# Kernel tuning notes

Hardware: AMD Instinct MI355X
Metric: run time of the kernel (lower is better)

Reference implementation:

```python
import jax, jax.numpy as jnp
import numpy as np

D = 512      # dim_model
F = 2048     # dim_feedforward
E = 8        # num_experts
K = 2        # num_experts_per_token
B, S = 2, 4096


def setup_inputs() -> dict:
    key = jax.random.key(0)
    ks = jax.random.split(key, 8)
    sd = 1.0 / np.sqrt(D)
    sf = 1.0 / np.sqrt(F)
    return {
        "x": jax.random.normal(ks[0], (B, S, D), dtype=jnp.float32),
        "router_w": jax.random.uniform(ks[1], (D, E), jnp.float32, -sd, sd),
        "router_b": jax.random.uniform(ks[2], (E,), jnp.float32, -sd, sd),
        "w1": jax.random.uniform(ks[3], (E, D, F), jnp.float32, -sd, sd),
        "b1": jax.random.uniform(ks[4], (E, F), jnp.float32, -sd, sd),
        "w2": jax.random.uniform(ks[5], (E, F, D), jnp.float32, -sf, sf),
        "b2": jax.random.uniform(ks[6], (E, D), jnp.float32, -sf, sf),
    }


def reference(x, router_w, router_b, w1, b1, w2, b2):
    orig_shape = x.shape
    flat = x.reshape(-1, orig_shape[-1])                     # [T, D]
    logits = flat @ router_w + router_b                      # [T, E]
    gates = jax.nn.softmax(logits, axis=-1)                  # [T, E]
    top_vals, top_idx = jax.lax.top_k(gates, K)              # [T, K]
    top_vals = top_vals / jnp.sum(top_vals, axis=-1, keepdims=True)
    # combine weight per (token, expert): zero for unselected experts,
    # so dense per-expert evaluation yields identical math to masked dispatch.
    onehot = jax.nn.one_hot(top_idx, E, dtype=flat.dtype)    # [T, K, E]
    comb = jnp.einsum('tk,tke->te', top_vals, onehot)        # [T, E]
    # expert FFNs over all tokens (dropout is identity in eval)
    hidden = jax.nn.relu(jnp.einsum('td,edf->etf', flat, w1) + b1[:, None, :])  # [E, T, F]
    eout = jnp.einsum('etf,efd->etd', hidden, w2) + b2[:, None, :]              # [E, T, D]
    out = jnp.einsum('te,etd->td', comb, eout)               # [T, D]
    return out.reshape(orig_shape)
```

## Files before the change

### kernel.cpp

```cpp
#include <hip/hip_runtime.h>
#include <cstdint>
#include <cstddef>

#define TD 512
#define TF 2048
#define NE 8
#define NT 8192
#define CAP 17408

using u16 = unsigned short;
using u32 = unsigned int;

typedef __attribute__((ext_vector_type(8))) __bf16 bf16x8;
typedef __attribute__((ext_vector_type(4))) float f32x4;

__device__ __forceinline__ u16 f2bf(float f) {
  u32 u = __float_as_uint(f);
  u32 r = (u + 0x7fffu + ((u >> 16) & 1u)) >> 16;
  return (u16)r;
}

__device__ __forceinline__ float bf2f(u16 b) {
  return __uint_as_float((u32)b << 16);
}

__device__ __forceinline__ void load_lds16(const void* g, void* l) {
  __builtin_amdgcn_global_load_lds(
      (const __attribute__((address_space(1))) void*)g,
      (__attribute__((address_space(3))) void*)l, 16, 0, 0);
}

__global__ void transpose_cvt_kernel(const float* __restrict__ in, u16* __restrict__ out,
                                     int R, int C) {
  __shared__ u16 tile[32][33];
  int c0 = blockIdx.x * 32, r0 = blockIdx.y * 32;
  const float* ib = in + (size_t)blockIdx.z * R * C;
  u16* ob = out + (size_t)blockIdx.z * R * C;
  #pragma unroll
  for (int rr = 0; rr < 32; rr += 8) {
    int r = r0 + threadIdx.y + rr;
    int c = c0 + threadIdx.x;
    tile[threadIdx.y + rr][threadIdx.x] = f2bf(ib[(size_t)r * C + c]);
  }
  __syncthreads();
  #pragma unroll
  for (int rr = 0; rr < 32; rr += 8) {
    int oc = c0 + threadIdx.y + rr;
    int orr = r0 + threadIdx.x;
    ob[(size_t)oc * R + orr] = tile[threadIdx.x][threadIdx.y + rr];
  }
}

__global__ void router_kernel(const float* __restrict__ x, const float* __restrict__ rw,
                              const float* __restrict__ rb, int2* __restrict__ tokE,
                              float2* __restrict__ tokG, u16* __restrict__ xb) {
  int wv = threadIdx.x >> 6;
  int lane = threadIdx.x & 63;
  int t = blockIdx.x * 4 + wv;
  const float* xr = x + (size_t)t * TD;
  float4 a0 = *reinterpret_cast<const float4*>(xr + lane * 4);
  float4 a1 = *reinterpret_cast<const float4*>(xr + 256 + lane * 4);
  {
    u16 o[8];
    o[0] = f2bf(a0.x); o[1] = f2bf(a0.y); o[2] = f2bf(a0.z); o[3] = f2bf(a0.w);
    o[4] = f2bf(a1.x); o[5] = f2bf(a1.y); o[6] = f2bf(a1.z); o[7] = f2bf(a1.w);
    u16* xo = xb + (size_t)t * TD;
    *reinterpret_cast<uint2*>(xo + lane * 4) = *reinterpret_cast<uint2*>(o);
    *reinterpret_cast<uint2*>(xo + 256 + lane * 4) = *reinterpret_cast<uint2*>(o + 4);
  }
  float p[NE];
  #pragma unroll
  for (int e = 0; e < NE; e++) p[e] = 0.f;
  float av[8] = {a0.x, a0.y, a0.z, a0.w, a1.x, a1.y, a1.z, a1.w};
  #pragma unroll
  for (int j = 0; j < 8; j++) {
    int d = (j < 4) ? (lane * 4 + j) : (256 + lane * 4 + j - 4);
    const float* r = rw + (size_t)d * NE;
    #pragma unroll
    for (int e = 0; e < NE; e++) p[e] += av[j] * r[e];
  }
  #pragma unroll
  for (int off = 32; off >= 1; off >>= 1) {
    #pragma unroll
    for (int e = 0; e < NE; e++) p[e] += __shfl_xor(p[e], off);
  }
  if (lane == 0) {
    float l[NE];
    #pragma unroll
    for (int e = 0; e < NE; e++) l[e] = p[e] + rb[e];
    float m = l[0];
    #pragma unroll
    for (int e = 1; e < NE; e++) m = fmaxf(m, l[e]);
    float g[NE];
    #pragma unroll
    for (int e = 0; e < NE; e++) g[e] = __expf(l[e] - m);
    int i0 = 0;
    #pragma unroll
    for (int e = 1; e < NE; e++) if (g[e] > g[i0]) i0 = e;
    int i1 = -1;
    #pragma unroll
    for (int e = 0; e < NE; e++) {
      if (e == i0) continue;
      if (i1 < 0 || g[e] > g[i1]) i1 = e;
    }
    float inv = 1.f / (g[i0] + g[i1]);
    tokE[t] = make_int2(i0, i1);
    tokG[t] = make_float2(g[i0] * inv, g[i1] * inv);
  }
}

__global__ void count_offsets_kernel(const int2* __restrict__ tokE, int* __restrict__ offs,
                                     int* __restrict__ cursors) {
  __shared__ int hist[NE];
  if (threadIdx.x < NE) {
    hist[threadIdx.x] = 0;
    cursors[threadIdx.x * 16] = 0;
  }
  __syncthreads();
  for (int t = threadIdx.x; t < NT; t += 1024) {
    int2 e = tokE[t];
    atomicAdd(&hist[e.x], 1);
    atomicAdd(&hist[e.y], 1);
  }
  __syncthreads();
  if (threadIdx.x == 0) {
    int tot = 0;
    for (int e = 0; e < NE; e++) {
      offs[e] = tot;
      tot += (hist[e] + 127) & ~127;
    }
    offs[NE] = tot;
  }
}

__global__ void fill_kernel(const int* __restrict__ offs, int* __restrict__ tok,
                            int* __restrict__ sexp) {
  int s = blockIdx.x * 256 + threadIdx.x;
  int e = NE - 1;
  #pragma unroll
  for (int i = 0; i < NE; i++)
    if (s >= offs[i] && s < offs[i + 1]) e = i;
  sexp[s] = e;
  tok[s] = -1;
}

__global__ void scatter_kernel(const int2* __restrict__ tokE,
                               const int* __restrict__ offs, int* __restrict__ cursors,
                               int* __restrict__ tok, int* __restrict__ slotOf) {
  int t = blockIdx.x * 256 + threadIdx.x;
  int lane = threadIdx.x & 63;
  int2 e = tokE[t];
  #pragma unroll
  for (int k = 0; k < 2; k++) {
    int ek = k ? e.y : e.x;
    #pragma unroll
    for (int ex = 0; ex < NE; ex++) {
      unsigned long long mask = __ballot(ek == ex);
      if (ek == ex) {
        int leader = __ffsll(mask) - 1;
        int rank = __popcll(mask & ((1ull << lane) - 1ull));
        int base = 0;
        if (lane == leader) base = atomicAdd(&cursors[ex * 16], __popcll(mask));
        base = __shfl(base, leader);
        int s = offs[ex] + base + rank;
        tok[s] = t;
        slotOf[t * 2 + k] = s;
      }
    }
  }
}

__global__ __launch_bounds__(256, 3) void gemm1_kernel(
    const u16* __restrict__ xb, const u16* __restrict__ w1t,
    const float* __restrict__ b1, const int* __restrict__ tok,
    const int* __restrict__ sexp, u16* __restrict__ H) {
  __shared__ u16 As[128 * 64];
  __shared__ u16 Bs[128 * 64];
  __shared__ int tokS[128];
  const int tid = threadIdx.x;
  const int s0 = blockIdx.x * 128;
  const int f0 = blockIdx.y * 128;
  const int e = sexp[s0];
  if (tid < 128) {
    int t = tok[s0 + tid];
    tokS[tid] = t < 0 ? 0 : t;
  }
  __syncthreads();

  const int lane = tid & 63;
  const int wv = tid >> 6;
  const int srow = lane >> 3;
  const int scol = (((lane & 7) ^ srow) & 7) * 8;
  const int wm = (wv >> 1) * 64;
  const int wn = (wv & 1) * 64;
  const int mrow = lane & 15;
  const int quad = lane >> 4;
  const int rq = mrow & 7;

  f32x4 zero = {0.f, 0.f, 0.f, 0.f};
  f32x4 acc[4][4];
  #pragma unroll
  for (int i = 0; i < 4; i++)
    #pragma unroll
    for (int j = 0; j < 4; j++) acc[i][j] = zero;

  const u16* bbase = w1t + ((size_t)e * TF + f0) * TD;

  for (int k0 = 0; k0 < TD; k0 += 64) {
    if (k0) __syncthreads();
    #pragma unroll
    for (int p = 0; p < 4; p++) {
      int row = wv * 32 + p * 8 + srow;
      load_lds16(xb + (size_t)tokS[row] * TD + k0 + scol, &As[(wv * 32 + p * 8) * 64]);
      load_lds16(bbase + (size_t)row * TD + k0 + scol, &Bs[(wv * 32 + p * 8) * 64]);
    }
    __syncthreads();
    #pragma unroll
    for (int ks = 0; ks < 2; ks++) {
      bf16x8 a[4], b[4];
      #pragma unroll
      for (int i = 0; i < 4; i++)
        a[i] = *reinterpret_cast<const bf16x8*>(
            &As[(wm + i * 16 + mrow) * 64 + ((ks * 4 + quad) ^ rq) * 8]);
      #pragma unroll
      for (int j = 0; j < 4; j++)
        b[j] = *reinterpret_cast<const bf16x8*>(
            &Bs[(wn + j * 16 + mrow) * 64 + ((ks * 4 + quad) ^ rq) * 8]);
      #pragma unroll
      for (int i = 0; i < 4; i++)
        #pragma unroll
        for (int j = 0; j < 4; j++)
          acc[i][j] = __builtin_amdgcn_mfma_f32_16x16x32_bf16(a[i], b[j], acc[i][j], 0, 0, 0);
    }
  }

  float bv[4];
  #pragma unroll
  for (int j = 0; j < 4; j++) bv[j] = b1[e * TF + f0 + wn + j * 16 + mrow];
  #pragma unroll
  for (int i = 0; i < 4; i++) {
    #pragma unroll
    for (int r = 0; r < 4; r++) {
      int row = s0 + wm + i * 16 + quad * 4 + r;
      u16* hrow = H + (size_t)row * TF + f0;
      #pragma unroll
      for (int j = 0; j < 4; j++) {
        float v = acc[i][j][r] + bv[j];
        v = v > 0.f ? v : 0.f;
        hrow[wn + j * 16 + mrow] = f2bf(v);
      }
    }
  }
}

__global__ __launch_bounds__(256, 3) void gemm2_kernel(
    const u16* __restrict__ H, const u16* __restrict__ w2t,
    const float* __restrict__ b2, const int* __restrict__ sexp,
    u16* __restrict__ eout) {
  __shared__ u16 As[128 * 64];
  __shared__ u16 Bs[128 * 64];
  const int tid = threadIdx.x;
  const int s0 = blockIdx.x * 128;
  const int d0 = blockIdx.y * 128;
  const int e = sexp[s0];

  const int lane = tid & 63;
  const int wv = tid >> 6;
  const int srow = lane >> 3;
  const int scol = (((lane & 7) ^ srow) & 7) * 8;
  const int wm = (wv >> 1) * 64;
  const int wn = (wv & 1) * 64;
  const int mrow = lane & 15;
  const int quad = lane >> 4;
  const int rq = mrow & 7;

  f32x4 zero = {0.f, 0.f, 0.f, 0.f};
  f32x4 acc[4][4];
  #pragma unroll
  for (int i = 0; i < 4; i++)
    #pragma unroll
    for (int j = 0; j < 4; j++) acc[i][j] = zero;

  const u16* bbase = w2t + ((size_t)e * TD + d0) * TF;

  for (int k0 = 0; k0 < TF; k0 += 64) {
    if (k0) __syncthreads();
    #pragma unroll
    for (int p = 0; p < 4; p++) {
      int row = wv * 32 + p * 8 + srow;
      load_lds16(H + (size_t)(s0 + row) * TF + k0 + scol, &As[(wv * 32 + p * 8) * 64]);
      load_lds16(bbase + (size_t)row * TF + k0 + scol, &Bs[(wv * 32 + p * 8) * 64]);
    }
    __syncthreads();
    #pragma unroll
    for (int ks = 0; ks < 2; ks++) {
      bf16x8 a[4], b[4];
      #pragma unroll
      for (int i = 0; i < 4; i++)
        a[i] = *reinterpret_cast<const bf16x8*>(
            &As[(wm + i * 16 + mrow) * 64 + ((ks * 4 + quad) ^ rq) * 8]);
      #pragma unroll
      for (int j = 0; j < 4; j++)
        b[j] = *reinterpret_cast<const bf16x8*>(
            &Bs[(wn + j * 16 + mrow) * 64 + ((ks * 4 + quad) ^ rq) * 8]);
      #pragma unroll
      for (int i = 0; i < 4; i++)
        #pragma unroll
        for (int j = 0; j < 4; j++)
          acc[i][j] = __builtin_amdgcn_mfma_f32_16x16x32_bf16(a[i], b[j], acc[i][j], 0, 0, 0);
    }
  }

  float bv[4];
  #pragma unroll
  for (int j = 0; j < 4; j++) bv[j] = b2[e * TD + d0 + wn + j * 16 + mrow];
  #pragma unroll
  for (int i = 0; i < 4; i++) {
    #pragma unroll
    for (int r = 0; r < 4; r++) {
      int row = s0 + wm + i * 16 + quad * 4 + r;
      u16* orow = eout + (size_t)row * TD + d0;
      #pragma unroll
      for (int j = 0; j < 4; j++) {
        orow[wn + j * 16 + mrow] = f2bf(acc[i][j][r] + bv[j]);
      }
    }
  }
}

__global__ void combine_kernel(const u16* __restrict__ eout, const int* __restrict__ slotOf,
                               const float2* __restrict__ tokG, float* __restrict__ out) {
  int wv = threadIdx.x >> 6;
  int lane = threadIdx.x & 63;
  int t = blockIdx.x * 4 + wv;
  int sA = slotOf[t * 2];
  int sB = slotOf[t * 2 + 1];
  float2 g = tokG[t];
  uint4 ua = *reinterpret_cast<const uint4*>(eout + (size_t)sA * TD + lane * 8);
  uint4 ub = *reinterpret_cast<const uint4*>(eout + (size_t)sB * TD + lane * 8);
  const u16* pa = reinterpret_cast<const u16*>(&ua);
  const u16* pb = reinterpret_cast<const u16*>(&ub);
  float o[8];
  #pragma unroll
  for (int k = 0; k < 8; k++) o[k] = g.x * bf2f(pa[k]) + g.y * bf2f(pb[k]);
  float* od = out + (size_t)t * TD + lane * 8;
  *reinterpret_cast<float4*>(od) = make_float4(o[0], o[1], o[2], o[3]);
  *reinterpret_cast<float4*>(od + 4) = make_float4(o[4], o[5], o[6], o[7]);
}

extern "C" void kernel_launch(void* const* d_in, const int* in_sizes, int n_in,
                              void* d_out, int out_size, void* d_ws, size_t ws_size,
                              hipStream_t stream) {
  const float* x  = (const float*)d_in[0];
  const float* rw = (const float*)d_in[1];
  const float* rb = (const float*)d_in[2];
  const float* w1 = (const float*)d_in[3];
  const float* b1 = (const float*)d_in[4];
  const float* w2 = (const float*)d_in[5];
  const float* b2 = (const float*)d_in[6];
  float* out = (float*)d_out;

  char* w = (char*)d_ws;
  u16* xb   = (u16*)w;            w += (size_t)NT * TD * 2;
  u16* w1t  = (u16*)w;            w += (size_t)NE * TD * TF * 2;
  u16* w2t  = (u16*)w;            w += (size_t)NE * TF * TD * 2;
  u16* H    = (u16*)w;            w += (size_t)CAP * TF * 2;
  u16* eout = (u16*)w;            w += (size_t)CAP * TD * 2;
  int* tok  = (int*)w;            w += (size_t)CAP * 4;
  int* sexp = (int*)w;            w += (size_t)CAP * 4;
  int* slotOf = (int*)w;          w += (size_t)NT * 2 * 4;
  int2* tokE = (int2*)w;          w += (size_t)NT * 8;
  float2* tokG = (float2*)w;      w += (size_t)NT * 8;
  int* cursors = (int*)w;         w += 1024;
  int* offs = (int*)w;            w += 256;

  transpose_cvt_kernel<<<dim3(TF / 32, TD / 32, NE), dim3(32, 8), 0, stream>>>(w1, w1t, TD, TF);
  transpose_cvt_kernel<<<dim3(TD / 32, TF / 32, NE), dim3(32, 8), 0, stream>>>(w2, w2t, TF, TD);
  router_kernel<<<dim3(NT / 4), dim3(256), 0, stream>>>(x, rw, rb, tokE, tokG, xb);
  count_offsets_kernel<<<dim3(1), dim3(1024), 0, stream>>>(tokE, offs, cursors);
  fill_kernel<<<dim3(CAP / 256), dim3(256), 0, stream>>>(offs, tok, sexp);
  scatter_kernel<<<dim3(NT / 256), dim3(256), 0, stream>>>(tokE, offs, cursors, tok, slotOf);
  gemm1_kernel<<<dim3(CAP / 128, TF / 128), dim3(256), 0, stream>>>(xb, w1t, b1, tok, sexp, H);
  gemm2_kernel<<<dim3(CAP / 128, TD / 128), dim3(256), 0, stream>>>(H, w2t, b2, sexp, eout);
  combine_kernel<<<dim3(NT / 4), dim3(256), 0, stream>>>(eout, slotOf, tokG, out);
}
```

Baseline: 268.8 us.

## Split-K gemm2, fuse weight transposes, drop fill kernel

Merges the two weight transpose/convert launches into one grid and removes the fill kernel. The GEMMs now derive each tile's expert from the offsets array, and gemm1 bounds-checks slots against per-expert counts instead of reading a -1 sentinel. gemm2 is split two ways along K to give more blocks (the before grid had only 136x4), writing two bf16 partial outputs that the combine kernel sums. This trades extra eout memory traffic and an extra bf16 rounding of the partials for better occupancy in gemm2 and fewer launches.

```diff
diff --git a/kernel.cpp b/kernel.cpp
--- a/kernel.cpp
+++ b/kernel.cpp
@@ -30,12 +30,9 @@
       (__attribute__((address_space(3))) void*)l, 16, 0, 0);
 }
 
-__global__ void transpose_cvt_kernel(const float* __restrict__ in, u16* __restrict__ out,
-                                     int R, int C) {
-  __shared__ u16 tile[32][33];
-  int c0 = blockIdx.x * 32, r0 = blockIdx.y * 32;
-  const float* ib = in + (size_t)blockIdx.z * R * C;
-  u16* ob = out + (size_t)blockIdx.z * R * C;
+__device__ __forceinline__ void transpose_tile(const float* __restrict__ ib,
+                                               u16* __restrict__ ob, int R, int C,
+                                               int r0, int c0, u16 (*tile)[33]) {
   #pragma unroll
   for (int rr = 0; rr < 32; rr += 8) {
     int r = r0 + threadIdx.y + rr;
@@ -48,6 +45,19 @@
     int oc = c0 + threadIdx.y + rr;
     int orr = r0 + threadIdx.x;
     ob[(size_t)oc * R + orr] = tile[threadIdx.x][threadIdx.y + rr];
+  }
+}
+
+__global__ void transpose_both_kernel(const float* __restrict__ w1, u16* __restrict__ w1t,
+                                      const float* __restrict__ w2, u16* __restrict__ w2t) {
+  __shared__ u16 tile[32][33];
+  int z = blockIdx.z;
+  if (z < 8) {
+    transpose_tile(w1 + (size_t)z * TD * TF, w1t + (size_t)z * TD * TF,
+                   TD, TF, blockIdx.y * 32, blockIdx.x * 32, tile);
+  } else {
+    transpose_tile(w2 + (size_t)(z - 8) * TF * TD, w2t + (size_t)(z - 8) * TF * TD,
+                   TF, TD, blockIdx.x * 32, blockIdx.y * 32, tile);
   }
 }
 
@@ -110,7 +120,7 @@
 }
 
 __global__ void count_offsets_kernel(const int2* __restrict__ tokE, int* __restrict__ offs,
-                                     int* __restrict__ cursors) {
+                                     int* __restrict__ cnt, int* __restrict__ cursors) {
   __shared__ int hist[NE];
   if (threadIdx.x < NE) {
     hist[threadIdx.x] = 0;
@@ -127,21 +137,11 @@
     int tot = 0;
     for (int e = 0; e < NE; e++) {
       offs[e] = tot;
+      cnt[e] = hist[e];
       tot += (hist[e] + 127) & ~127;
     }
     offs[NE] = tot;
   }
-}
-
-__global__ void fill_kernel(const int* __restrict__ offs, int* __restrict__ tok,
-                            int* __restrict__ sexp) {
-  int s = blockIdx.x * 256 + threadIdx.x;
-  int e = NE - 1;
-  #pragma unroll
-  for (int i = 0; i < NE; i++)
-    if (s >= offs[i] && s < offs[i + 1]) e = i;
-  sexp[s] = e;
-  tok[s] = -1;
 }
 
 __global__ void scatter_kernel(const int2* __restrict__ tokE,
@@ -173,17 +173,22 @@
 __global__ __launch_bounds__(256, 3) void gemm1_kernel(
     const u16* __restrict__ xb, const u16* __restrict__ w1t,
     const float* __restrict__ b1, const int* __restrict__ tok,
-    const int* __restrict__ sexp, u16* __restrict__ H) {
+    const int* __restrict__ offs, const int* __restrict__ cnt,
+    u16* __restrict__ H) {
   __shared__ u16 As[128 * 64];
   __shared__ u16 Bs[128 * 64];
   __shared__ int tokS[128];
   const int tid = threadIdx.x;
   const int s0 = blockIdx.x * 128;
   const int f0 = blockIdx.y * 128;
-  const int e = sexp[s0];
+  int e = 0;
+  #pragma unroll
+  for (int i = 1; i <= 7; i++)
+    if (s0 >= offs[i]) e = i;
+  const int vend = offs[e] + cnt[e];
   if (tid < 128) {
-    int t = tok[s0 + tid];
-    tokS[tid] = t < 0 ? 0 : t;
+    int s = s0 + tid;
+    tokS[tid] = (s < vend) ? tok[s] : 0;
   }
   __syncthreads();
 
@@ -255,14 +260,18 @@
 
 __global__ __launch_bounds__(256, 3) void gemm2_kernel(
     const u16* __restrict__ H, const u16* __restrict__ w2t,
-    const float* __restrict__ b2, const int* __restrict__ sexp,
-    u16* __restrict__ eout) {
+    const float* __restrict__ b2, const int* __restrict__ offs,
+    u16* __restrict__ eoutP) {
   __shared__ u16 As[128 * 64];
   __shared__ u16 Bs[128 * 64];
   const int tid = threadIdx.x;
-  const int s0 = blockIdx.x * 128;
-  const int d0 = blockIdx.y * 128;
-  const int e = sexp[s0];
+  const int d0 = blockIdx.x * 128;
+  const int s0 = blockIdx.y * 128;
+  const int kz = blockIdx.z;
+  int e = 0;
+  #pragma unroll
+  for (int i = 1; i <= 7; i++)
+    if (s0 >= offs[i]) e = i;
 
   const int lane = tid & 63;
   const int wv = tid >> 6;
@@ -282,9 +291,11 @@
     for (int j = 0; j < 4; j++) acc[i][j] = zero;
 
   const u16* bbase = w2t + ((size_t)e * TD + d0) * TF;
-
-  for (int k0 = 0; k0 < TF; k0 += 64) {
-    if (k0) __syncthreads();
+  const int kbeg = kz * (TF / 2);
+  const int kend = kbeg + (TF / 2);
+
+  for (int k0 = kbeg; k0 < kend; k0 += 64) {
+    if (k0 != kbeg) __syncthreads();
     #pragma unroll
     for (int p = 0; p < 4; p++) {
       int row = wv * 32 + p * 8 + srow;
@@ -313,13 +324,15 @@
 
   float bv[4];
   #pragma unroll
-  for (int j = 0; j < 4; j++) bv[j] = b2[e * TD + d0 + wn + j * 16 + mrow];
+  for (int j = 0; j < 4; j++)
+    bv[j] = (kz == 0) ? b2[e * TD + d0 + wn + j * 16 + mrow] : 0.f;
+  u16* base = eoutP + (size_t)kz * CAP * TD;
   #pragma unroll
   for (int i = 0; i < 4; i++) {
     #pragma unroll
     for (int r = 0; r < 4; r++) {
       int row = s0 + wm + i * 16 + quad * 4 + r;
-      u16* orow = eout + (size_t)row * TD + d0;
+      u16* orow = base + (size_t)row * TD + d0;
       #pragma unroll
       for (int j = 0; j < 4; j++) {
         orow[wn + j * 16 + mrow] = f2bf(acc[i][j][r] + bv[j]);
@@ -328,7 +341,7 @@
   }
 }
 
-__global__ void combine_kernel(const u16* __restrict__ eout, const int* __restrict__ slotOf,
+__global__ void combine_kernel(const u16* __restrict__ eoutP, const int* __restrict__ slotOf,
                                const float2* __restrict__ tokG, float* __restrict__ out) {
   int wv = threadIdx.x >> 6;
   int lane = threadIdx.x & 63;
@@ -336,13 +349,20 @@
   int sA = slotOf[t * 2];
   int sB = slotOf[t * 2 + 1];
   float2 g = tokG[t];
-  uint4 ua = *reinterpret_cast<const uint4*>(eout + (size_t)sA * TD + lane * 8);
-  uint4 ub = *reinterpret_cast<const uint4*>(eout + (size_t)sB * TD + lane * 8);
-  const u16* pa = reinterpret_cast<const u16*>(&ua);
-  const u16* pb = reinterpret_cast<const u16*>(&ub);
+  const u16* P0 = eoutP;
+  const u16* P1 = eoutP + (size_t)CAP * TD;
+  uint4 ua0 = *reinterpret_cast<const uint4*>(P0 + (size_t)sA * TD + lane * 8);
+  uint4 ua1 = *reinterpret_cast<const uint4*>(P1 + (size_t)sA * TD + lane * 8);
+  uint4 ub0 = *reinterpret_cast<const uint4*>(P0 + (size_t)sB * TD + lane * 8);
+  uint4 ub1 = *reinterpret_cast<const uint4*>(P1 + (size_t)sB * TD + lane * 8);
+  const u16* pa0 = reinterpret_cast<const u16*>(&ua0);
+  const u16* pa1 = reinterpret_cast<const u16*>(&ua1);
+  const u16* pb0 = reinterpret_cast<const u16*>(&ub0);
+  const u16* pb1 = reinterpret_cast<const u16*>(&ub1);
   float o[8];
   #pragma unroll
-  for (int k = 0; k < 8; k++) o[k] = g.x * bf2f(pa[k]) + g.y * bf2f(pb[k]);
+  for (int k = 0; k < 8; k++)
+    o[k] = g.x * (bf2f(pa0[k]) + bf2f(pa1[k])) + g.y * (bf2f(pb0[k]) + bf2f(pb1[k]));
   float* od = out + (size_t)t * TD + lane * 8;
   *reinterpret_cast<float4*>(od) = make_float4(o[0], o[1], o[2], o[3]);
   *reinterpret_cast<float4*>(od + 4) = make_float4(o[4], o[5], o[6], o[7]);
@@ -361,26 +381,24 @@
   float* out = (float*)d_out;
 
   char* w = (char*)d_ws;
-  u16* xb   = (u16*)w;            w += (size_t)NT * TD * 2;
-  u16* w1t  = (u16*)w;            w += (size_t)NE * TD * TF * 2;
-  u16* w2t  = (u16*)w;            w += (size_t)NE * TF * TD * 2;
-  u16* H    = (u16*)w;            w += (size_t)CAP * TF * 2;
-  u16* eout = (u16*)w;            w += (size_t)CAP * TD * 2;
-  int* tok  = (int*)w;            w += (size_t)CAP * 4;
-  int* sexp = (int*)w;            w += (size_t)CAP * 4;
+  u16* xb    = (u16*)w;           w += (size_t)NT * TD * 2;
+  u16* w1t   = (u16*)w;           w += (size_t)NE * TD * TF * 2;
+  u16* w2t   = (u16*)w;           w += (size_t)NE * TF * TD * 2;
+  u16* H     = (u16*)w;           w += (size_t)CAP * TF * 2;
+  u16* eoutP = (u16*)w;           w += (size_t)2 * CAP * TD * 2;
+  int* tok   = (int*)w;           w += (size_t)CAP * 4;
   int* slotOf = (int*)w;          w += (size_t)NT * 2 * 4;
   int2* tokE = (int2*)w;          w += (size_t)NT * 8;
   float2* tokG = (float2*)w;      w += (size_t)NT * 8;
   int* cursors = (int*)w;         w += 1024;
-  int* offs = (int*)w;            w += 256;
-
-  transpose_cvt_kernel<<<dim3(TF / 32, TD / 32, NE), dim3(32, 8), 0, stream>>>(w1, w1t, TD, TF);
-  transpose_cvt_kernel<<<dim3(TD / 32, TF / 32, NE), dim3(32, 8), 0, stream>>>(w2, w2t, TF, TD);
+  int* offs  = (int*)w;           w += 256;
+  int* cnt   = (int*)w;           w += 256;
+
+  transpose_both_kernel<<<dim3(64, 16, 16), dim3(32, 8), 0, stream>>>(w1, w1t, w2, w2t);
   router_kernel<<<dim3(NT / 4), dim3(256), 0, stream>>>(x, rw, rb, tokE, tokG, xb);
-  count_offsets_kernel<<<dim3(1), dim3(1024), 0, stream>>>(tokE, offs, cursors);
-  fill_kernel<<<dim3(CAP / 256), dim3(256), 0, stream>>>(offs, tok, sexp);
+  count_offsets_kernel<<<dim3(1), dim3(1024), 0, stream>>>(tokE, offs, cnt, cursors);
   scatter_kernel<<<dim3(NT / 256), dim3(256), 0, stream>>>(tokE, offs, cursors, tok, slotOf);
-  gemm1_kernel<<<dim3(CAP / 128, TF / 128), dim3(256), 0, stream>>>(xb, w1t, b1, tok, sexp, H);
-  gemm2_kernel<<<dim3(CAP / 128, TD / 128), dim3(256), 0, stream>>>(H, w2t, b2, sexp, eout);
-  combine_kernel<<<dim3(NT / 4), dim3(256), 0, stream>>>(eout, slotOf, tokG, out);
-}
+  gemm1_kernel<<<dim3(CAP / 128, TF / 128), dim3(256), 0, stream>>>(xb, w1t, b1, tok, offs, cnt, H);
+  gemm2_kernel<<<dim3(TD / 128, CAP / 128, 2), dim3(256), 0, stream>>>(H, w2t, b2, offs, eoutP);
+  combine_kernel<<<dim3(NT / 4), dim3(256), 0, stream>>>(eoutP, slotOf, tokG, out);
+}
```

After: 268.0 us. No clear change (-0.3%).

## Fuse weight transposes and router into one prep kernel, parallelize histogram, drop fill pass

Applied to the files above, without the earlier changes.

Merges the two weight transpose-convert kernels and the router into a single launch, with the transposes now using 64x64 tiles and vectorized float4 loads and uint2 stores. The single-block count kernel becomes a 32-block histogram that uses a last-block-done atomic to compute offsets and per-expert counts. The fill kernel is removed: the GEMMs derive the expert from the offsets and mask padded slots using the counts. This cuts launch count and serial work, at the cost of relying on the threadfence/atomic last-block pattern being correct.

```diff
diff --git a/kernel.cpp b/kernel.cpp
--- a/kernel.cpp
+++ b/kernel.cpp
@@ -30,118 +30,140 @@
       (__attribute__((address_space(3))) void*)l, 16, 0, 0);
 }
 
-__global__ void transpose_cvt_kernel(const float* __restrict__ in, u16* __restrict__ out,
-                                     int R, int C) {
-  __shared__ u16 tile[32][33];
-  int c0 = blockIdx.x * 32, r0 = blockIdx.y * 32;
-  const float* ib = in + (size_t)blockIdx.z * R * C;
-  u16* ob = out + (size_t)blockIdx.z * R * C;
-  #pragma unroll
-  for (int rr = 0; rr < 32; rr += 8) {
-    int r = r0 + threadIdx.y + rr;
-    int c = c0 + threadIdx.x;
-    tile[threadIdx.y + rr][threadIdx.x] = f2bf(ib[(size_t)r * C + c]);
+__device__ __forceinline__ void transpose64(const float* __restrict__ ib,
+                                            u16* __restrict__ ob, int R, int C,
+                                            int r0, int c0, u16* tile ) {
+  const int tid = threadIdx.x;
+  const int l16 = tid & 15;
+  const int grp = tid >> 4;
+  #pragma unroll
+  for (int p = 0; p < 4; p++) {
+    int r = p * 16 + grp;
+    float4 v = *reinterpret_cast<const float4*>(ib + (size_t)(r0 + r) * C + c0 + l16 * 4);
+    u16 o[4] = {f2bf(v.x), f2bf(v.y), f2bf(v.z), f2bf(v.w)};
+    *reinterpret_cast<uint2*>(&tile[r * 68 + l16 * 4]) = *reinterpret_cast<uint2*>(o);
   }
   __syncthreads();
   #pragma unroll
-  for (int rr = 0; rr < 32; rr += 8) {
-    int oc = c0 + threadIdx.y + rr;
-    int orr = r0 + threadIdx.x;
-    ob[(size_t)oc * R + orr] = tile[threadIdx.x][threadIdx.y + rr];
-  }
-}
-
-__global__ void router_kernel(const float* __restrict__ x, const float* __restrict__ rw,
-                              const float* __restrict__ rb, int2* __restrict__ tokE,
-                              float2* __restrict__ tokG, u16* __restrict__ xb) {
-  int wv = threadIdx.x >> 6;
-  int lane = threadIdx.x & 63;
-  int t = blockIdx.x * 4 + wv;
-  const float* xr = x + (size_t)t * TD;
-  float4 a0 = *reinterpret_cast<const float4*>(xr + lane * 4);
-  float4 a1 = *reinterpret_cast<const float4*>(xr + 256 + lane * 4);
-  {
-    u16 o[8];
-    o[0] = f2bf(a0.x); o[1] = f2bf(a0.y); o[2] = f2bf(a0.z); o[3] = f2bf(a0.w);
-    o[4] = f2bf(a1.x); o[5] = f2bf(a1.y); o[6] = f2bf(a1.z); o[7] = f2bf(a1.w);
-    u16* xo = xb + (size_t)t * TD;
-    *reinterpret_cast<uint2*>(xo + lane * 4) = *reinterpret_cast<uint2*>(o);
-    *reinterpret_cast<uint2*>(xo + 256 + lane * 4) = *reinterpret_cast<uint2*>(o + 4);
-  }
-  float p[NE];
-  #pragma unroll
-  for (int e = 0; e < NE; e++) p[e] = 0.f;
-  float av[8] = {a0.x, a0.y, a0.z, a0.w, a1.x, a1.y, a1.z, a1.w};
-  #pragma unroll
-  for (int j = 0; j < 8; j++) {
-    int d = (j < 4) ? (lane * 4 + j) : (256 + lane * 4 + j - 4);
-    const float* r = rw + (size_t)d * NE;
-    #pragma unroll
-    for (int e = 0; e < NE; e++) p[e] += av[j] * r[e];
-  }
-  #pragma unroll
-  for (int off = 32; off >= 1; off >>= 1) {
-    #pragma unroll
-    for (int e = 0; e < NE; e++) p[e] += __shfl_xor(p[e], off);
-  }
-  if (lane == 0) {
-    float l[NE];
-    #pragma unroll
-    for (int e = 0; e < NE; e++) l[e] = p[e] + rb[e];
-    float m = l[0];
-    #pragma unroll
-    for (int e = 1; e < NE; e++) m = fmaxf(m, l[e]);
-    float g[NE];
-    #pragma unroll
-    for (int e = 0; e < NE; e++) g[e] = __expf(l[e] - m);
-    int i0 = 0;
-    #pragma unroll
-    for (int e = 1; e < NE; e++) if (g[e] > g[i0]) i0 = e;
-    int i1 = -1;
-    #pragma unroll
-    for (int e = 0; e < NE; e++) {
-      if (e == i0) continue;
-      if (i1 < 0 || g[e] > g[i1]) i1 = e;
-    }
-    float inv = 1.f / (g[i0] + g[i1]);
-    tokE[t] = make_int2(i0, i1);
-    tokG[t] = make_float2(g[i0] * inv, g[i1] * inv);
-  }
-}
-
-__global__ void count_offsets_kernel(const int2* __restrict__ tokE, int* __restrict__ offs,
-                                     int* __restrict__ cursors) {
-  __shared__ int hist[NE];
-  if (threadIdx.x < NE) {
-    hist[threadIdx.x] = 0;
-    cursors[threadIdx.x * 16] = 0;
-  }
+  for (int p = 0; p < 4; p++) {
+    int c = p * 16 + grp;
+    int rr = l16 * 4;
+    u16 o[4] = {tile[(rr + 0) * 68 + c], tile[(rr + 1) * 68 + c],
+                tile[(rr + 2) * 68 + c], tile[(rr + 3) * 68 + c]};
+    *reinterpret_cast<uint2*>(ob + (size_t)(c0 + c) * R + r0 + rr) = *reinterpret_cast<uint2*>(o);
+  }
+}
+
+__global__ void prep_kernel(const float* __restrict__ x, const float* __restrict__ rw,
+                            const float* __restrict__ rb, int2* __restrict__ tokE,
+                            float2* __restrict__ tokG, u16* __restrict__ xb,
+                            const float* __restrict__ w1, u16* __restrict__ w1t,
+                            const float* __restrict__ w2, u16* __restrict__ w2t,
+                            int* __restrict__ ghist) {
+  __shared__ u16 tile[64 * 68];
+  int b = blockIdx.x;
+  if (b < NT / 4) {
+    if (b == 0 && threadIdx.x < 16) ghist[threadIdx.x] = 0;
+    int wv = threadIdx.x >> 6;
+    int lane = threadIdx.x & 63;
+    int t = b * 4 + wv;
+    const float* xr = x + (size_t)t * TD;
+    float4 a0 = *reinterpret_cast<const float4*>(xr + lane * 4);
+    float4 a1 = *reinterpret_cast<const float4*>(xr + 256 + lane * 4);
+    {
+      u16 o[8];
+      o[0] = f2bf(a0.x); o[1] = f2bf(a0.y); o[2] = f2bf(a0.z); o[3] = f2bf(a0.w);
+      o[4] = f2bf(a1.x); o[5] = f2bf(a1.y); o[6] = f2bf(a1.z); o[7] = f2bf(a1.w);
+      u16* xo = xb + (size_t)t * TD;
+      *reinterpret_cast<uint2*>(xo + lane * 4) = *reinterpret_cast<uint2*>(o);
+      *reinterpret_cast<uint2*>(xo + 256 + lane * 4) = *reinterpret_cast<uint2*>(o + 4);
+    }
+    float p[NE];
+    #pragma unroll
+    for (int e = 0; e < NE; e++) p[e] = 0.f;
+    float av[8] = {a0.x, a0.y, a0.z, a0.w, a1.x, a1.y, a1.z, a1.w};
+    #pragma unroll
+    for (int j = 0; j < 8; j++) {
+      int d = (j < 4) ? (lane * 4 + j) : (256 + lane * 4 + j - 4);
+      const float* r = rw + (size_t)d * NE;
+      #pragma unroll
+      for (int e = 0; e < NE; e++) p[e] += av[j] * r[e];
+    }
+    #pragma unroll
+    for (int off = 32; off >= 1; off >>= 1) {
+      #pragma unroll
+      for (int e = 0; e < NE; e++) p[e] += __shfl_xor(p[e], off);
+    }
+    if (lane == 0) {
+      float l[NE];
+      #pragma unroll
+      for (int e = 0; e < NE; e++) l[e] = p[e] + rb[e];
+      float m = l[0];
+      #pragma unroll
+      for (int e = 1; e < NE; e++) m = fmaxf(m, l[e]);
+      float g[NE];
+      #pragma unroll
+      for (int e = 0; e < NE; e++) g[e] = __expf(l[e] - m);
+      int i0 = 0;
+      #pragma unroll
+      for (int e = 1; e < NE; e++) if (g[e] > g[i0]) i0 = e;
+      int i1 = -1;
+      #pragma unroll
+      for (int e = 0; e < NE; e++) {
+        if (e == i0) continue;
+        if (i1 < 0 || g[e] > g[i1]) i1 = e;
+      }
+      float inv = 1.f / (g[i0] + g[i1]);
+      tokE[t] = make_int2(i0, i1);
+      tokG[t] = make_float2(g[i0] * inv, g[i1] * inv);
+    }
+  } else {
+    int tb = b - NT / 4;
+    int which = tb >> 11;
+    int idx = tb & 2047;
+    int e = idx >> 8;
+    int tl = idx & 255;
+    if (which == 0) {
+      int rt = tl >> 5, ct = tl & 31;
+      transpose64(w1 + (size_t)e * TD * TF, w1t + (size_t)e * TD * TF,
+                  TD, TF, rt * 64, ct * 64, tile);
+    } else {
+      int rt = tl >> 3, ct = tl & 7;
+      transpose64(w2 + (size_t)e * TF * TD, w2t + (size_t)e * TF * TD,
+                  TF, TD, rt * 64, ct * 64, tile);
+    }
+  }
+}
+
+__global__ void hist_kernel(const int2* __restrict__ tokE, int* __restrict__ ghist,
+                            int* __restrict__ offs, int* __restrict__ cnt,
+                            int* __restrict__ cursors) {
+  __shared__ int h[NE];
+  __shared__ int last;
+  if (threadIdx.x < NE) h[threadIdx.x] = 0;
   __syncthreads();
-  for (int t = threadIdx.x; t < NT; t += 1024) {
-    int2 e = tokE[t];
-    atomicAdd(&hist[e.x], 1);
-    atomicAdd(&hist[e.y], 1);
-  }
+  int t = blockIdx.x * 256 + threadIdx.x;
+  int2 e = tokE[t];
+  atomicAdd(&h[e.x], 1);
+  atomicAdd(&h[e.y], 1);
   __syncthreads();
-  if (threadIdx.x == 0) {
-    int tot = 0;
-    for (int e = 0; e < NE; e++) {
-      offs[e] = tot;
-      tot += (hist[e] + 127) & ~127;
-    }
-    offs[NE] = tot;
-  }
-}
-
-__global__ void fill_kernel(const int* __restrict__ offs, int* __restrict__ tok,
-                            int* __restrict__ sexp) {
-  int s = blockIdx.x * 256 + threadIdx.x;
-  int e = NE - 1;
-  #pragma unroll
-  for (int i = 0; i < NE; i++)
-    if (s >= offs[i] && s < offs[i + 1]) e = i;
-  sexp[s] = e;
-  tok[s] = -1;
+  if (threadIdx.x < NE) atomicAdd(&ghist[threadIdx.x], h[threadIdx.x]);
+  __threadfence();
+  if (threadIdx.x == 0) last = (atomicAdd(&ghist[15], 1) == 31);
+  __syncthreads();
+  if (last) {
+    if (threadIdx.x == 0) {
+      int tot = 0;
+      for (int i = 0; i < NE; i++) {
+        int hv = atomicAdd(&ghist[i], 0);
+        offs[i] = tot;
+        cnt[i] = hv;
+        tot += (hv + 127) & ~127;
+      }
+      offs[NE] = tot;
+    }
+    if (threadIdx.x < NE) cursors[threadIdx.x * 16] = 0;
+  }
 }
 
 __global__ void scatter_kernel(const int2* __restrict__ tokE,
@@ -173,17 +195,22 @@
 __global__ __launch_bounds__(256, 3) void gemm1_kernel(
     const u16* __restrict__ xb, const u16* __restrict__ w1t,
     const float* __restrict__ b1, const int* __restrict__ tok,
-    const int* __restrict__ sexp, u16* __restrict__ H) {
+    const int* __restrict__ offs, const int* __restrict__ cnt,
+    u16* __restrict__ H) {
   __shared__ u16 As[128 * 64];
   __shared__ u16 Bs[128 * 64];
   __shared__ int tokS[128];
   const int tid = threadIdx.x;
   const int s0 = blockIdx.x * 128;
   const int f0 = blockIdx.y * 128;
-  const int e = sexp[s0];
+  int e = 0;
+  #pragma unroll
+  for (int i = 1; i <= 7; i++)
+    if (s0 >= offs[i]) e = i;
+  const int vend = offs[e] + cnt[e];
   if (tid < 128) {
-    int t = tok[s0 + tid];
-    tokS[tid] = t < 0 ? 0 : t;
+    int s = s0 + tid;
+    tokS[tid] = (s < vend) ? tok[s] : 0;
   }
   __syncthreads();
 
@@ -255,14 +282,17 @@
 
 __global__ __launch_bounds__(256, 3) void gemm2_kernel(
     const u16* __restrict__ H, const u16* __restrict__ w2t,
-    const float* __restrict__ b2, const int* __restrict__ sexp,
+    const float* __restrict__ b2, const int* __restrict__ offs,
     u16* __restrict__ eout) {
   __shared__ u16 As[128 * 64];
   __shared__ u16 Bs[128 * 64];
   const int tid = threadIdx.x;
   const int s0 = blockIdx.x * 128;
   const int d0 = blockIdx.y * 128;
-  const int e = sexp[s0];
+  int e = 0;
+  #pragma unroll
+  for (int i = 1; i <= 7; i++)
+    if (s0 >= offs[i]) e = i;
 
   const int lane = tid & 63;
   const int wv = tid >> 6;
@@ -361,26 +391,25 @@
   float* out = (float*)d_out;
 
   char* w = (char*)d_ws;
-  u16* xb   = (u16*)w;            w += (size_t)NT * TD * 2;
-  u16* w1t  = (u16*)w;            w += (size_t)NE * TD * TF * 2;
-  u16* w2t  = (u16*)w;            w += (size_t)NE * TF * TD * 2;
-  u16* H    = (u16*)w;            w += (size_t)CAP * TF * 2;
-  u16* eout = (u16*)w;            w += (size_t)CAP * TD * 2;
-  int* tok  = (int*)w;            w += (size_t)CAP * 4;
-  int* sexp = (int*)w;            w += (size_t)CAP * 4;
+  u16* xb    = (u16*)w;           w += (size_t)NT * TD * 2;
+  u16* w1t   = (u16*)w;           w += (size_t)NE * TD * TF * 2;
+  u16* w2t   = (u16*)w;           w += (size_t)NE * TF * TD * 2;
+  u16* H     = (u16*)w;           w += (size_t)CAP * TF * 2;
+  u16* eout  = (u16*)w;           w += (size_t)CAP * TD * 2;
+  int* tok   = (int*)w;           w += (size_t)CAP * 4;
   int* slotOf = (int*)w;          w += (size_t)NT * 2 * 4;
   int2* tokE = (int2*)w;          w += (size_t)NT * 8;
   float2* tokG = (float2*)w;      w += (size_t)NT * 8;
+  int* ghist = (int*)w;           w += 256;
   int* cursors = (int*)w;         w += 1024;
-  int* offs = (int*)w;            w += 256;
-
-  transpose_cvt_kernel<<<dim3(TF / 32, TD / 32, NE), dim3(32, 8), 0, stream>>>(w1, w1t, TD, TF);
-  transpose_cvt_kernel<<<dim3(TD / 32, TF / 32, NE), dim3(32, 8), 0, stream>>>(w2, w2t, TF, TD);
-  router_kernel<<<dim3(NT / 4), dim3(256), 0, stream>>>(x, rw, rb, tokE, tokG, xb);
-  count_offsets_kernel<<<dim3(1), dim3(1024), 0, stream>>>(tokE, offs, cursors);
-  fill_kernel<<<dim3(CAP / 256), dim3(256), 0, stream>>>(offs, tok, sexp);
+  int* offs  = (int*)w;           w += 256;
+  int* cnt   = (int*)w;           w += 256;
+
+  prep_kernel<<<dim3(NT / 4 + 4096), dim3(256), 0, stream>>>(
+      x, rw, rb, tokE, tokG, xb, w1, w1t, w2, w2t, ghist);
+  hist_kernel<<<dim3(32), dim3(256), 0, stream>>>(tokE, ghist, offs, cnt, cursors);
   scatter_kernel<<<dim3(NT / 256), dim3(256), 0, stream>>>(tokE, offs, cursors, tok, slotOf);
-  gemm1_kernel<<<dim3(CAP / 128, TF / 128), dim3(256), 0, stream>>>(xb, w1t, b1, tok, sexp, H);
-  gemm2_kernel<<<dim3(CAP / 128, TD / 128), dim3(256), 0, stream>>>(H, w2t, b2, sexp, eout);
+  gemm1_kernel<<<dim3(CAP / 128, TF / 128), dim3(256), 0, stream>>>(xb, w1t, b1, tok, offs, cnt, H);
+  gemm2_kernel<<<dim3(CAP / 128, TD / 128), dim3(256), 0, stream>>>(H, w2t, b2, offs, eout);
   combine_kernel<<<dim3(NT / 4), dim3(256), 0, stream>>>(eout, slotOf, tokG, out);
 }
```

Result: no change. 267.2 us (-0.6%).
